# Kernel optimization log

Hardware: AMD Instinct MI355X
Metric: run time of the kernel (lower is better)

Reference implementation:

```python
import jax, jax.numpy as jnp
import numpy as np

B, S, C, H = 1024, 254, 2, 1024
TIME_DIM = 64
HALF = TIME_DIM // 2
N_STEPS = 50


def time_embed(t):
    # t: [B] -> [B, 64] sinusoidal embedding, matching SinusoidalEmbedding(64)
    freqs = jnp.exp(jnp.arange(HALF, dtype=jnp.float32) * (-np.log(10000.0) / (HALF - 1)))
    ang = t[:, None] * freqs[None, :]  # [B, 32]
    return jnp.concatenate([jnp.sin(ang), jnp.cos(ang)], axis=-1)  # [B, 64]


def setup_inputs() -> dict:
    key = jax.random.key(0)
    ks = jax.random.split(key, 12)
    inp = {}
    inp["state"] = jax.random.normal(ks[0], (B, S), jnp.float32)
    inp["x0"] = jax.random.normal(ks[1], (B, C), jnp.float32)  # initial noise of sample()
    dims = [S + C + TIME_DIM, H, H, H, H, C]  # 320 -> 1024 x4 -> 2
    for i in range(5):
        kw, kb = jax.random.split(ks[2 + i])
        inp[f"W{i}"] = jax.random.normal(kw, (dims[i], dims[i + 1]), jnp.float32) * (1.0 / np.sqrt(dims[i]))
        inp[f"b{i}"] = jax.random.normal(kb, (dims[i + 1],), jnp.float32) * 0.01
    return inp


def reference(state, x0, W0, b0, W1, b1, W2, b2, W3, b3, W4, b4):
    dt = 1.0 / N_STEPS

    def velocity(x, t):
        temb = time_embed(t)
        h = jnp.concatenate([state, x, temb], axis=-1)  # [B, 320]
        h = jax.nn.silu(h @ W0 + b0)
        h = jax.nn.silu(h @ W1 + b1)
        h = jax.nn.silu(h @ W2 + b2)
        h = jax.nn.silu(h @ W3 + b3)
        return h @ W4 + b4  # [B, C]

    def step(x, i):
        t = jnp.full((state.shape[0],), i * dt, dtype=jnp.float32)
        return x + dt * velocity(x, t), None

    x, _ = jax.lax.scan(step, x0, jnp.arange(N_STEPS, dtype=jnp.float32))
    return x
```

## Files before the change

kernel.cpp:

```cpp
#include <hip/hip_runtime.h>


typedef __bf16 bf16x8 __attribute__((ext_vector_type(8)));
typedef float  f32x4  __attribute__((ext_vector_type(4)));
typedef float  f32x2  __attribute__((ext_vector_type(2)));
typedef unsigned short u16;
typedef u16 u16x8 __attribute__((ext_vector_type(8)));
typedef u16 u16x4 __attribute__((ext_vector_type(4)));
typedef u16 u16x2 __attribute__((ext_vector_type(2)));

#define H 1024
#define BATCH 1024
#define SDIM 254
#define NSTEP 50
#define DT 0.02f

__device__ __forceinline__ u16 f2bf(float f) {
  unsigned int u = __float_as_uint(f);
  return (u16)((u + 0x7FFFu + ((u >> 16) & 1u)) >> 16);
}

__device__ __forceinline__ float silu(float v) {
  return v / (1.0f + __expf(-v));
}

__global__ void transpose_w(const float* __restrict__ A, const float* __restrict__ B,
                            const float* __restrict__ C, u16* __restrict__ TA,
                            u16* __restrict__ TB, u16* __restrict__ TC) {
  const float* W = (blockIdx.z == 0) ? A : (blockIdx.z == 1) ? B : C;
  u16* T = (blockIdx.z == 0) ? TA : (blockIdx.z == 1) ? TB : TC;
  __shared__ float tile[32][33];
  const int n0 = blockIdx.x * 32, k0 = blockIdx.y * 32;
  const int tx = threadIdx.x & 31, ty = threadIdx.x >> 5;
#pragma unroll
  for (int i = 0; i < 4; ++i)
    tile[ty + 8 * i][tx] = W[(k0 + ty + 8 * i) * H + n0 + tx];
  __syncthreads();
#pragma unroll
  for (int i = 0; i < 4; ++i)
    T[(size_t)(n0 + ty + 8 * i) * H + k0 + tx] = f2bf(tile[tx][ty + 8 * i]);
}

__global__ __launch_bounds__(256) void base_gemm(const float* __restrict__ state,
                                                 const float* __restrict__ W0,
                                                 const float* __restrict__ b0,
                                                 float* __restrict__ base) {
  __shared__ float Sst[64][68];
  __shared__ float Wl[64][68];
  const int bc = blockIdx.x, br = blockIdx.y, tid = threadIdx.x;
  const int myrow = (tid >> 4) * 4;
  const int mycol = (tid & 15) * 4;
  const int lr = tid >> 2;
  const int lc = (tid & 3) * 16;
  f32x4 acc[4] = {};

  for (int kc = 0; kc < 4; ++kc) {
    const int k0 = kc * 64;
#pragma unroll
    for (int j = 0; j < 8; ++j) {
      const int k = k0 + lc + 2 * j;
      float vx = 0.f, vy = 0.f;
      if (k + 1 < SDIM) {
        float2 v = *(const float2*)&state[(size_t)(br * 64 + lr) * SDIM + k];
        vx = v.x; vy = v.y;
      } else if (k < SDIM) {
        vx = state[(size_t)(br * 64 + lr) * SDIM + k];
      }
      Sst[lr][lc + 2 * j] = vx;
      Sst[lr][lc + 2 * j + 1] = vy;
    }
#pragma unroll
    for (int j = 0; j < 4; ++j) {
      f32x4 wv = {};
      if (k0 + lr < SDIM)
        wv = *(const f32x4*)&W0[(size_t)(k0 + lr) * H + bc * 64 + lc + 4 * j];
      *(f32x4*)&Wl[lr][lc + 4 * j] = wv;
    }
    __syncthreads();
#pragma unroll 4
    for (int kk = 0; kk < 64; kk += 4) {
      f32x4 sv[4], wv[4];
#pragma unroll
      for (int r = 0; r < 4; ++r) sv[r] = *(const f32x4*)&Sst[myrow + r][kk];
#pragma unroll
      for (int j = 0; j < 4; ++j) wv[j] = *(const f32x4*)&Wl[kk + j][mycol];
#pragma unroll
      for (int r = 0; r < 4; ++r)
#pragma unroll
        for (int j = 0; j < 4; ++j)
          acc[r] += sv[r][j] * wv[j];
    }
    __syncthreads();
  }

  const f32x4 bv = *(const f32x4*)&b0[bc * 64 + mycol];
#pragma unroll
  for (int r = 0; r < 4; ++r) {
    f32x4 o = acc[r] + bv;
    *(f32x4*)&base[(size_t)(br * 64 + myrow + r) * H + bc * 64 + mycol] = o;
  }
}

__global__ void tvec_kernel(const float* __restrict__ W0, float* __restrict__ tvec) {
  const int s = blockIdx.x;
  const int h = blockIdx.y * 256 + threadIdx.x;
  const float t = (float)s * DT;
  float acc = 0.0f;
#pragma unroll
  for (int j = 0; j < 32; ++j) {
    float fr = __expf((float)j * (-9.210340371976184f / 31.0f));
    float ang = t * fr;
    acc += __sinf(ang) * W0[(256 + j) * H + h] + __cosf(ang) * W0[(288 + j) * H + h];
  }
  tvec[s * H + h] = acc;
}

__global__ void init_kernel(const float* __restrict__ base, const float* __restrict__ tvec,
                            const float* __restrict__ x0, const float* __restrict__ W0,
                            u16* __restrict__ h0, float* __restrict__ xout) {
  const int b = blockIdx.x, tid = threadIdx.x;
  const float xa = x0[2 * b], xb = x0[2 * b + 1];
  if (tid == 0) { xout[2 * b] = xa; xout[2 * b + 1] = xb; }
  const int n = tid * 4;
  float4 bs = *(const float4*)&base[(size_t)b * H + n];
  float4 tv = *(const float4*)&tvec[n];
  float4 wa = *(const float4*)&W0[254 * H + n];
  float4 wb = *(const float4*)&W0[255 * H + n];
  u16x4 r;
  r[0] = f2bf(silu(bs.x + tv.x + xa * wa.x + xb * wb.x));
  r[1] = f2bf(silu(bs.y + tv.y + xa * wa.y + xb * wb.y));
  r[2] = f2bf(silu(bs.z + tv.z + xa * wa.z + xb * wb.z));
  r[3] = f2bf(silu(bs.w + tv.w + xa * wa.w + xb * wb.w));
  *(u16x4*)&h0[(size_t)b * H + n] = r;
}

__global__ __launch_bounds__(512, 2) void gemm_mfma(const u16* __restrict__ A,
                                                    const u16* __restrict__ BT,
                                                    const float* __restrict__ bias,
                                                    void* __restrict__ out, int out_bf16) {
  __shared__ float red[8][16][68];
  const int tid = threadIdx.x;
  const int w = tid >> 6, lane = tid & 63;
  const int lr = lane & 15, quad = lane >> 4;
  const int bn = blockIdx.x, bm = blockIdx.y;

  const u16* Ap = A + (size_t)(bm * 64 + lr) * H + w * 128 + quad * 8;
  const u16* Bp = BT + (size_t)(bn * 64 + lr) * H + w * 128 + quad * 8;

  bf16x8 fa[4][4], fb[4][4];
#pragma unroll
  for (int it = 0; it < 4; ++it)
#pragma unroll
    for (int q = 0; q < 4; ++q) {
      fa[it][q] = *(const bf16x8*)(Ap + q * 16 * H + it * 32);
      fb[it][q] = *(const bf16x8*)(Bp + q * 16 * H + it * 32);
    }

  f32x4 acc[4][4] = {};
#pragma unroll
  for (int it = 0; it < 4; ++it)
#pragma unroll
    for (int mt = 0; mt < 4; ++mt)
#pragma unroll
      for (int nt = 0; nt < 4; ++nt)
        acc[mt][nt] = __builtin_amdgcn_mfma_f32_16x16x32_bf16(fa[it][mt], fb[it][nt],
                                                              acc[mt][nt], 0, 0, 0);

  const int m = tid >> 5;
  const int n0 = (tid & 31) * 2;
  const f32x2 bv = *(const f32x2*)&bias[bn * 64 + n0];
#pragma unroll
  for (int p = 0; p < 4; ++p) {
    if (p) __syncthreads();
#pragma unroll
    for (int nt = 0; nt < 4; ++nt)
#pragma unroll
      for (int r = 0; r < 4; ++r)
        red[w][quad * 4 + r][nt * 16 + lr] = acc[p][nt][r];
    __syncthreads();
    f32x2 s = {};
#pragma unroll
    for (int ww = 0; ww < 8; ++ww) s += *(const f32x2*)&red[ww][m][n0];
    const int gm = bm * 64 + p * 16 + m;
    const float v0 = silu(s[0] + bv[0]);
    const float v1 = silu(s[1] + bv[1]);
    if (out_bf16) {
      u16x2 o = {f2bf(v0), f2bf(v1)};
      *(u16x2*)&((u16*)out)[(size_t)gm * H + bn * 64 + n0] = o;
    } else {
      f32x2 o = {v0, v1};
      *(f32x2*)&((float*)out)[(size_t)gm * H + bn * 64 + n0] = o;
    }
  }
}

__global__ void tail_kernel(const float* __restrict__ h3, const float* __restrict__ W4,
                            const float* __restrict__ b4, float* __restrict__ x,
                            const float* __restrict__ base, const float* __restrict__ tvec,
                            const float* __restrict__ W0, u16* __restrict__ h0, int s) {
  const int b = blockIdx.x, tid = threadIdx.x;
  float s0 = 0.0f, s1 = 0.0f;
  for (int h = tid; h < H; h += 256) {
    float v = h3[(size_t)b * H + h];
    s0 += v * W4[2 * h];
    s1 += v * W4[2 * h + 1];
  }
#pragma unroll
  for (int o = 32; o > 0; o >>= 1) {
    s0 += __shfl_down(s0, o);
    s1 += __shfl_down(s1, o);
  }
  __shared__ float red[8];
  __shared__ float xs[2];
  const int w = tid >> 6;
  if ((tid & 63) == 0) { red[w * 2] = s0; red[w * 2 + 1] = s1; }
  __syncthreads();
  if (tid == 0) {
    float v0 = red[0] + red[2] + red[4] + red[6] + b4[0];
    float v1 = red[1] + red[3] + red[5] + red[7] + b4[1];
    float xa = x[2 * b] + DT * v0;
    float xb = x[2 * b + 1] + DT * v1;
    x[2 * b] = xa; x[2 * b + 1] = xb;
    xs[0] = xa; xs[1] = xb;
  }
  __syncthreads();
  if (s < NSTEP - 1) {
    const float xa = xs[0], xb = xs[1];
    const int n = tid * 4;
    float4 bs = *(const float4*)&base[(size_t)b * H + n];
    float4 tv = *(const float4*)&tvec[(size_t)(s + 1) * H + n];
    float4 wa = *(const float4*)&W0[254 * H + n];
    float4 wb = *(const float4*)&W0[255 * H + n];
    u16x4 r;
    r[0] = f2bf(silu(bs.x + tv.x + xa * wa.x + xb * wb.x));
    r[1] = f2bf(silu(bs.y + tv.y + xa * wa.y + xb * wb.y));
    r[2] = f2bf(silu(bs.z + tv.z + xa * wa.z + xb * wb.z));
    r[3] = f2bf(silu(bs.w + tv.w + xa * wa.w + xb * wb.w));
    *(u16x4*)&h0[(size_t)b * H + n] = r;
  }
}

extern "C" void kernel_launch(void* const* d_in, const int* in_sizes, int n_in,
                              void* d_out, int out_size, void* d_ws, size_t ws_size,
                              hipStream_t stream) {
  const float* state = (const float*)d_in[0];
  const float* x0    = (const float*)d_in[1];
  const float* W0    = (const float*)d_in[2];
  const float* b0    = (const float*)d_in[3];
  const float* W1    = (const float*)d_in[4];
  const float* b1    = (const float*)d_in[5];
  const float* W2    = (const float*)d_in[6];
  const float* b2    = (const float*)d_in[7];
  const float* W3    = (const float*)d_in[8];
  const float* b3    = (const float*)d_in[9];
  const float* W4    = (const float*)d_in[10];
  const float* b4    = (const float*)d_in[11];
  float* xout = (float*)d_out;

  char* ws = (char*)d_ws;
  const size_t MB = 1024 * 1024;
  float* base = (float*)(ws + 0);
  float* h3f  = (float*)(ws + 4 * MB);
  float* tvec = (float*)(ws + 8 * MB);
  u16* w1t = (u16*)(ws + 8 * MB + 256 * 1024);
  u16* w2t = (u16*)(ws + 10 * MB + 256 * 1024);
  u16* w3t = (u16*)(ws + 12 * MB + 256 * 1024);
  u16* hA  = (u16*)(ws + 14 * MB + 256 * 1024);
  u16* hB  = (u16*)(ws + 16 * MB + 256 * 1024);
  u16* hC  = (u16*)(ws + 18 * MB + 256 * 1024);

  transpose_w<<<dim3(32, 32, 3), 256, 0, stream>>>(W1, W2, W3, w1t, w2t, w3t);
  base_gemm<<<dim3(16, 16), 256, 0, stream>>>(state, W0, b0, base);
  tvec_kernel<<<dim3(NSTEP, 4), 256, 0, stream>>>(W0, tvec);
  init_kernel<<<BATCH, 256, 0, stream>>>(base, tvec, x0, W0, hA, xout);

  for (int s = 0; s < NSTEP; ++s) {
    gemm_mfma<<<dim3(16, 16), 512, 0, stream>>>(hA, w1t, b1, hB, 1);
    gemm_mfma<<<dim3(16, 16), 512, 0, stream>>>(hB, w2t, b2, hC, 1);
    gemm_mfma<<<dim3(16, 16), 512, 0, stream>>>(hC, w3t, b3, h3f, 0);
    tail_kernel<<<BATCH, 256, 0, stream>>>(h3f, W4, b4, xout, base, tvec, W0, hA, s);
  }
}
```

Measured before the change: 2.013 ms.

## Replace per-step kernel launches with a persistent kernel using grid barriers

Measured after the change: 7.042 ms. 3.5x slower.

```diff
diff --git a/kernel.cpp b/kernel.cpp
--- a/kernel.cpp
+++ b/kernel.cpp
@@ -115,128 +115,184 @@
   tvec[s * H + h] = acc;
 }
 
-__global__ void init_kernel(const float* __restrict__ base, const float* __restrict__ tvec,
-                            const float* __restrict__ x0, const float* __restrict__ W0,
-                            u16* __restrict__ h0, float* __restrict__ xout) {
-  const int b = blockIdx.x, tid = threadIdx.x;
-  const float xa = x0[2 * b], xb = x0[2 * b + 1];
-  if (tid == 0) { xout[2 * b] = xa; xout[2 * b + 1] = xb; }
-  const int n = tid * 4;
-  float4 bs = *(const float4*)&base[(size_t)b * H + n];
-  float4 tv = *(const float4*)&tvec[n];
-  float4 wa = *(const float4*)&W0[254 * H + n];
-  float4 wb = *(const float4*)&W0[255 * H + n];
-  u16x4 r;
-  r[0] = f2bf(silu(bs.x + tv.x + xa * wa.x + xb * wb.x));
-  r[1] = f2bf(silu(bs.y + tv.y + xa * wa.y + xb * wb.y));
-  r[2] = f2bf(silu(bs.z + tv.z + xa * wa.z + xb * wb.z));
-  r[3] = f2bf(silu(bs.w + tv.w + xa * wa.w + xb * wb.w));
-  *(u16x4*)&h0[(size_t)b * H + n] = r;
-}
-
-__global__ __launch_bounds__(512, 2) void gemm_mfma(const u16* __restrict__ A,
-                                                    const u16* __restrict__ BT,
-                                                    const float* __restrict__ bias,
-                                                    void* __restrict__ out, int out_bf16) {
+__global__ void bar_init(unsigned int* __restrict__ bar) {
+  bar[threadIdx.x] = 0u;
+  bar[threadIdx.x + 256] = 0u;
+  bar[threadIdx.x + 512] = 0u;
+  bar[threadIdx.x + 768] = 0u;
+}
+
+__device__ __forceinline__ void gsync(unsigned int* bar, unsigned int phase) {
+  __syncthreads();
+  if (threadIdx.x == 0) {
+    __threadfence();
+    unsigned int* leaf = bar + (blockIdx.x << 5);
+    unsigned int v = __hip_atomic_fetch_add(leaf, 1u, __ATOMIC_ACQ_REL,
+                                            __HIP_MEMORY_SCOPE_AGENT);
+    if (v == phase * 16u - 1u) {
+      unsigned int r = __hip_atomic_fetch_add(bar + 512, 1u, __ATOMIC_ACQ_REL,
+                                              __HIP_MEMORY_SCOPE_AGENT);
+      if (r == phase * 16u - 1u)
+        __hip_atomic_store(bar + 544, phase, __ATOMIC_RELEASE,
+                           __HIP_MEMORY_SCOPE_AGENT);
+    }
+    while (__hip_atomic_load(bar + 544, __ATOMIC_ACQUIRE,
+                             __HIP_MEMORY_SCOPE_AGENT) < phase)
+      __builtin_amdgcn_s_sleep(2);
+    __threadfence();
+  }
+  __syncthreads();
+}
+
+template <int TAIL>
+__device__ __forceinline__ void layer_phase(const u16* __restrict__ A,
+                                            const u16* __restrict__ BT,
+                                            const float* __restrict__ bias,
+                                            u16* __restrict__ outp,
+                                            const float* __restrict__ W4,
+                                            float* __restrict__ vpart,
+                                            int bn, int bm, int w, int lane, int tid,
+                                            float (*red)[16][68]) {
+  const int lr = lane & 15, quad = lane >> 4;
+  const u16* Ap = A + (size_t)(bm * 64 + lr) * H + w * 128 + quad * 8;
+  const u16* Bp = BT + (size_t)(bn * 64 + lr) * H + w * 128 + quad * 8;
+
+  bf16x8 fa[4][4], fb[4][4];
+#pragma unroll
+  for (int it = 0; it < 4; ++it)
+#pragma unroll
+    for (int q = 0; q < 4; ++q) {
+      fa[it][q] = *(const bf16x8*)(Ap + q * 16 * H + it * 32);
+      fb[it][q] = *(const bf16x8*)(Bp + q * 16 * H + it * 32);
+    }
+
+  f32x4 acc[4][4] = {};
+#pragma unroll
+  for (int it = 0; it < 4; ++it)
+#pragma unroll
+    for (int mt = 0; mt < 4; ++mt)
+#pragma unroll
+      for (int nt = 0; nt < 4; ++nt)
+        acc[mt][nt] = __builtin_amdgcn_mfma_f32_16x16x32_bf16(fa[it][mt], fb[it][nt],
+                                                              acc[mt][nt], 0, 0, 0);
+
+  const int m = tid >> 5, n0 = (tid & 31) * 2;
+  const f32x2 bv = *(const f32x2*)&bias[bn * 64 + n0];
+  f32x4 w4v = {};
+  if (TAIL) w4v = *(const f32x4*)&W4[2 * (bn * 64 + n0)];
+#pragma unroll
+  for (int p = 0; p < 4; ++p) {
+    if (p) __syncthreads();
+#pragma unroll
+    for (int nt = 0; nt < 4; ++nt)
+#pragma unroll
+      for (int r = 0; r < 4; ++r)
+        red[w][quad * 4 + r][nt * 16 + lr] = acc[p][nt][r];
+    __syncthreads();
+    f32x2 sv = {};
+#pragma unroll
+    for (int ww = 0; ww < 8; ++ww) sv += *(const f32x2*)&red[ww][m][n0];
+    const int gm = bm * 64 + p * 16 + m;
+    if (!TAIL) {
+      u16x2 o = {f2bf(silu(sv[0] + bv[0])), f2bf(silu(sv[1] + bv[1]))};
+      *(u16x2*)&outp[(size_t)gm * H + bn * 64 + n0] = o;
+    } else {
+      const float t0 = silu(sv[0] + bv[0]), t1 = silu(sv[1] + bv[1]);
+      float pv0 = t0 * w4v[0] + t1 * w4v[2];
+      float pv1 = t0 * w4v[1] + t1 * w4v[3];
+#pragma unroll
+      for (int o = 16; o > 0; o >>= 1) {
+        pv0 += __shfl_xor(pv0, o);
+        pv1 += __shfl_xor(pv1, o);
+      }
+      if ((tid & 31) == 0) {
+        float2 pr = {pv0, pv1};
+        *(float2*)&vpart[(size_t)(bn * 1024 + gm) * 2] = pr;
+      }
+    }
+  }
+}
+
+__global__ __launch_bounds__(512, 2) void persist(
+    const float* __restrict__ x0, const float* __restrict__ base,
+    const float* __restrict__ tvec, const float* __restrict__ W0,
+    const float* __restrict__ b1, const float* __restrict__ b2,
+    const float* __restrict__ b3, const float* __restrict__ b4,
+    const float* __restrict__ W4,
+    const u16* __restrict__ w1t, const u16* __restrict__ w2t,
+    const u16* __restrict__ w3t,
+    u16* __restrict__ hA, u16* __restrict__ hB, u16* __restrict__ hC,
+    float* __restrict__ vpart, float* __restrict__ xping,
+    unsigned int* __restrict__ bar, float* __restrict__ xout) {
   __shared__ float red[8][16][68];
   const int tid = threadIdx.x;
   const int w = tid >> 6, lane = tid & 63;
-  const int lr = lane & 15, quad = lane >> 4;
   const int bn = blockIdx.x, bm = blockIdx.y;
-
-  const u16* Ap = A + (size_t)(bm * 64 + lr) * H + w * 128 + quad * 8;
-  const u16* Bp = BT + (size_t)(bn * 64 + lr) * H + w * 128 + quad * 8;
-
-  bf16x8 fa[4][4], fb[4][4];
-#pragma unroll
-  for (int it = 0; it < 4; ++it)
-#pragma unroll
-    for (int q = 0; q < 4; ++q) {
-      fa[it][q] = *(const bf16x8*)(Ap + q * 16 * H + it * 32);
-      fb[it][q] = *(const bf16x8*)(Bp + q * 16 * H + it * 32);
-    }
-
-  f32x4 acc[4][4] = {};
-#pragma unroll
-  for (int it = 0; it < 4; ++it)
-#pragma unroll
-    for (int mt = 0; mt < 4; ++mt)
-#pragma unroll
-      for (int nt = 0; nt < 4; ++nt)
-        acc[mt][nt] = __builtin_amdgcn_mfma_f32_16x16x32_bf16(fa[it][mt], fb[it][nt],
-                                                              acc[mt][nt], 0, 0, 0);
-
-  const int m = tid >> 5;
-  const int n0 = (tid & 31) * 2;
-  const f32x2 bv = *(const f32x2*)&bias[bn * 64 + n0];
-#pragma unroll
-  for (int p = 0; p < 4; ++p) {
-    if (p) __syncthreads();
-#pragma unroll
-    for (int nt = 0; nt < 4; ++nt)
-#pragma unroll
-      for (int r = 0; r < 4; ++r)
-        red[w][quad * 4 + r][nt * 16 + lr] = acc[p][nt][r];
-    __syncthreads();
-    f32x2 s = {};
-#pragma unroll
-    for (int ww = 0; ww < 8; ++ww) s += *(const f32x2*)&red[ww][m][n0];
-    const int gm = bm * 64 + p * 16 + m;
-    const float v0 = silu(s[0] + bv[0]);
-    const float v1 = silu(s[1] + bv[1]);
-    if (out_bf16) {
-      u16x2 o = {f2bf(v0), f2bf(v1)};
-      *(u16x2*)&((u16*)out)[(size_t)gm * H + bn * 64 + n0] = o;
-    } else {
-      f32x2 o = {v0, v1};
-      *(f32x2*)&((float*)out)[(size_t)gm * H + bn * 64 + n0] = o;
-    }
-  }
-}
-
-__global__ void tail_kernel(const float* __restrict__ h3, const float* __restrict__ W4,
-                            const float* __restrict__ b4, float* __restrict__ x,
-                            const float* __restrict__ base, const float* __restrict__ tvec,
-                            const float* __restrict__ W0, u16* __restrict__ h0, int s) {
-  const int b = blockIdx.x, tid = threadIdx.x;
-  float s0 = 0.0f, s1 = 0.0f;
-  for (int h = tid; h < H; h += 256) {
-    float v = h3[(size_t)b * H + h];
-    s0 += v * W4[2 * h];
-    s1 += v * W4[2 * h + 1];
-  }
-#pragma unroll
-  for (int o = 32; o > 0; o >>= 1) {
-    s0 += __shfl_down(s0, o);
-    s1 += __shfl_down(s1, o);
-  }
-  __shared__ float red[8];
-  __shared__ float xs[2];
-  const int w = tid >> 6;
-  if ((tid & 63) == 0) { red[w * 2] = s0; red[w * 2 + 1] = s1; }
-  __syncthreads();
-  if (tid == 0) {
-    float v0 = red[0] + red[2] + red[4] + red[6] + b4[0];
-    float v1 = red[1] + red[3] + red[5] + red[7] + b4[1];
-    float xa = x[2 * b] + DT * v0;
-    float xb = x[2 * b + 1] + DT * v1;
-    x[2 * b] = xa; x[2 * b + 1] = xb;
-    xs[0] = xa; xs[1] = xb;
-  }
-  __syncthreads();
-  if (s < NSTEP - 1) {
-    const float xa = xs[0], xb = xs[1];
-    const int n = tid * 4;
-    float4 bs = *(const float4*)&base[(size_t)b * H + n];
-    float4 tv = *(const float4*)&tvec[(size_t)(s + 1) * H + n];
-    float4 wa = *(const float4*)&W0[254 * H + n];
-    float4 wb = *(const float4*)&W0[255 * H + n];
-    u16x4 r;
-    r[0] = f2bf(silu(bs.x + tv.x + xa * wa.x + xb * wb.x));
-    r[1] = f2bf(silu(bs.y + tv.y + xa * wa.y + xb * wb.y));
-    r[2] = f2bf(silu(bs.z + tv.z + xa * wa.z + xb * wb.z));
-    r[3] = f2bf(silu(bs.w + tv.w + xa * wa.w + xb * wb.w));
-    *(u16x4*)&h0[(size_t)b * H + n] = r;
+  unsigned int phase = 0;
+
+#pragma unroll 1
+  for (int s = 0; s < NSTEP; ++s) {
+    {
+      const int r = tid >> 3, c0 = (tid & 7) * 8;
+      const int gr = bm * 64 + r;
+      float xa, xb;
+      if (s == 0) {
+        xa = x0[2 * gr];
+        xb = x0[2 * gr + 1];
+      } else {
+        float va = b4[0], vb = b4[1];
+#pragma unroll 4
+        for (int j = 0; j < 16; ++j) {
+          float2 pp = *(const float2*)&vpart[(size_t)(j * 1024 + gr) * 2];
+          va += pp.x; vb += pp.y;
+        }
+        float2 xo = *(const float2*)&xping[((s - 1) & 1) * 2048 + 2 * gr];
+        xa = xo.x + DT * va;
+        xb = xo.y + DT * vb;
+      }
+      if (bn == 0 && (tid & 7) == 0) {
+        float2 xn = {xa, xb};
+        *(float2*)&xping[(s & 1) * 2048 + 2 * gr] = xn;
+      }
+      const int gc = bn * 64 + c0;
+      const float* bp = &base[(size_t)gr * H + gc];
+      const float* tp = &tvec[(size_t)s * H + gc];
+      const float* wap = &W0[254 * H + gc];
+      const float* wbp = &W0[255 * H + gc];
+      u16x8 o;
+#pragma unroll
+      for (int jj = 0; jj < 2; ++jj) {
+        f32x4 bs = *(const f32x4*)(bp + 4 * jj);
+        f32x4 tv = *(const f32x4*)(tp + 4 * jj);
+        f32x4 wa = *(const f32x4*)(wap + 4 * jj);
+        f32x4 wb = *(const f32x4*)(wbp + 4 * jj);
+#pragma unroll
+        for (int e = 0; e < 4; ++e)
+          o[4 * jj + e] = f2bf(silu(bs[e] + tv[e] + xa * wa[e] + xb * wb[e]));
+      }
+      *(u16x8*)&hA[(size_t)gr * H + gc] = o;
+    }
+    gsync(bar, ++phase);
+
+    layer_phase<0>(hA, w1t, b1, hB, nullptr, nullptr, bn, bm, w, lane, tid, red);
+    gsync(bar, ++phase);
+    layer_phase<0>(hB, w2t, b2, hC, nullptr, nullptr, bn, bm, w, lane, tid, red);
+    gsync(bar, ++phase);
+    layer_phase<1>(hC, w3t, b3, nullptr, W4, vpart, bn, bm, w, lane, tid, red);
+    gsync(bar, ++phase);
+  }
+
+  if (bn == 0 && (tid & 7) == 0) {
+    const int gr = bm * 64 + (tid >> 3);
+    float va = b4[0], vb = b4[1];
+#pragma unroll 4
+    for (int j = 0; j < 16; ++j) {
+      float2 pp = *(const float2*)&vpart[(size_t)(j * 1024 + gr) * 2];
+      va += pp.x; vb += pp.y;
+    }
+    float2 xo = *(const float2*)&xping[2048 + 2 * gr];
+    xout[2 * gr] = xo.x + DT * va;
+    xout[2 * gr + 1] = xo.y + DT * vb;
   }
 }
 
@@ -259,25 +315,25 @@
 
   char* ws = (char*)d_ws;
   const size_t MB = 1024 * 1024;
+  const size_t KB = 1024;
   float* base = (float*)(ws + 0);
-  float* h3f  = (float*)(ws + 4 * MB);
-  float* tvec = (float*)(ws + 8 * MB);
-  u16* w1t = (u16*)(ws + 8 * MB + 256 * 1024);
-  u16* w2t = (u16*)(ws + 10 * MB + 256 * 1024);
-  u16* w3t = (u16*)(ws + 12 * MB + 256 * 1024);
-  u16* hA  = (u16*)(ws + 14 * MB + 256 * 1024);
-  u16* hB  = (u16*)(ws + 16 * MB + 256 * 1024);
-  u16* hC  = (u16*)(ws + 18 * MB + 256 * 1024);
+  float* tvec = (float*)(ws + 4 * MB);
+  u16* w1t = (u16*)(ws + 4 * MB + 256 * KB);
+  u16* w2t = (u16*)(ws + 6 * MB + 256 * KB);
+  u16* w3t = (u16*)(ws + 8 * MB + 256 * KB);
+  u16* hA  = (u16*)(ws + 10 * MB + 256 * KB);
+  u16* hB  = (u16*)(ws + 12 * MB + 256 * KB);
+  u16* hC  = (u16*)(ws + 14 * MB + 256 * KB);
+  float* vpart = (float*)(ws + 16 * MB + 256 * KB);
+  float* xping = (float*)(ws + 16 * MB + 384 * KB);
+  unsigned int* bar = (unsigned int*)(ws + 16 * MB + 400 * KB);
 
   transpose_w<<<dim3(32, 32, 3), 256, 0, stream>>>(W1, W2, W3, w1t, w2t, w3t);
   base_gemm<<<dim3(16, 16), 256, 0, stream>>>(state, W0, b0, base);
   tvec_kernel<<<dim3(NSTEP, 4), 256, 0, stream>>>(W0, tvec);
-  init_kernel<<<BATCH, 256, 0, stream>>>(base, tvec, x0, W0, hA, xout);
-
-  for (int s = 0; s < NSTEP; ++s) {
-    gemm_mfma<<<dim3(16, 16), 512, 0, stream>>>(hA, w1t, b1, hB, 1);
-    gemm_mfma<<<dim3(16, 16), 512, 0, stream>>>(hB, w2t, b2, hC, 1);
-    gemm_mfma<<<dim3(16, 16), 512, 0, stream>>>(hC, w3t, b3, h3f, 0);
-    tail_kernel<<<BATCH, 256, 0, stream>>>(h3f, W4, b4, xout, base, tvec, W0, hA, s);
-  }
-}
+  bar_init<<<1, 256, 0, stream>>>(bar);
+
+  persist<<<dim3(16, 16), 512, 0, stream>>>(x0, base, tvec, W0, b1, b2, b3, b4,
+                                            W4, w1t, w2t, w3t, hA, hB, hC,
+                                            vpart, xping, bar, xout);
+}
```
